# Kernel tuning notes

Hardware: AMD Instinct MI355X
Metric: run time of the kernel (lower is better)

Reference implementation:

```python
import jax, jax.numpy as jnp
import numpy as np

H = 512
N = 512
BSZ = 8
L = 4096
DIRECTION = 2  # 0=forward, 1=backward, 2=bidirectional (split N in half)


def setup_inputs() -> dict:
    key = jax.random.key(0)
    k = jax.random.split(key, 6)
    u = jax.random.normal(k[0], (BSZ, L, H), jnp.float32)
    # variable lengths in [L//2, L]
    lengths = jax.random.randint(k[1], (BSZ,), L // 2, L + 1).astype(jnp.int32)
    # LRU init: r_min=0, r_max=1, max_phase=2*pi
    u1 = jax.random.uniform(k[2], (N,), jnp.float32)
    nu_log = jnp.log(-0.5 * jnp.log(u1))
    u2 = jax.random.uniform(k[3], (N,), jnp.float32)
    theta_log = jnp.log(2.0 * np.pi * u2)
    lam = jnp.exp(-jnp.exp(nu_log) + 1j * jnp.exp(theta_log))  # (N,) complex
    gamma = jnp.sqrt(1.0 - jnp.abs(lam) ** 2)[:, None]          # (N,1)
    B = jax.random.normal(k[4], (H, N, 2), jnp.float32) / np.float32(np.sqrt(2 * H)) * gamma
    C = jax.random.normal(k[5], (2, H, N), jnp.float32) / np.float32(np.sqrt(N))
    return {"u": u, "lengths": lengths, "nu_log": nu_log, "theta_log": theta_log, "B": B, "C": C}


def _lru_scan(lam, Bu, reverse):
    """Diagonal linear recurrence x_t = lam * x_{t-1} + Bu_t along axis 2 via associative scan.
    lam: (n,) complex; Bu: (B, n, L) complex."""
    a = jnp.broadcast_to(lam[None, :, None], Bu.shape)

    def op(e1, e2):
        a1, b1 = e1
        a2, b2 = e2
        return a1 * a2, a2 * b1 + b2

    _, x = jax.lax.associative_scan(op, (a, Bu), axis=2, reverse=reverse)
    return x


def reference(u, lengths, nu_log, theta_log, B, C):
    lam = jnp.exp(-jnp.exp(nu_log) + 1j * jnp.exp(theta_log))  # (N,)
    Bc = B[..., 0] + 1j * B[..., 1]                            # (H, N) complex
    Bu = jnp.einsum('blh,hn->bnl', u, Bc)                      # (B, N, L) complex
    mask = jnp.arange(L)[None, :] < lengths[:, None]           # (B, L)
    Bu = Bu * mask[:, None, :]
    if DIRECTION == 2:
        h = N // 2
        x = jnp.concatenate([
            _lru_scan(lam[:h], Bu[:, :h], reverse=False),
            _lru_scan(lam[h:], Bu[:, h:], reverse=True),
        ], axis=1)
    elif DIRECTION == 0:
        x = _lru_scan(lam, Bu, reverse=False)
    else:
        x = _lru_scan(lam, Bu, reverse=True)
    x = x * mask[:, None, :]           # zero outputs past each sequence length
    x = jnp.swapaxes(x, 1, 2)          # (B, L, N)
    y = x.real @ C[0] - x.imag @ C[1]  # (B, L, H)  (requires H == N, as in source)
    return y
```

## Files before the change

### kernel.cpp

```cpp
#include <hip/hip_runtime.h>

#define L_SEQ   4096
#define BSZQ    8
#define ROWS    (BSZQ * L_SEQ)
#define KC1     512
#define NC1     1024
#define KC2     1024
#define NC2     512
#define CHUNK   64
#define NCHUNK  64

typedef __attribute__((ext_vector_type(8))) short bfrag;
typedef __attribute__((ext_vector_type(4))) float ffrag;

static __device__ __forceinline__ unsigned short f2bf(float f) {
    union { float f; unsigned int u; } v; v.f = f;
    unsigned int r = v.u + 0x7fffu + ((v.u >> 16) & 1u);
    return (unsigned short)(r >> 16);
}
static __device__ __forceinline__ unsigned int pk2(float a, float b) {
    return (unsigned int)f2bf(a) | ((unsigned int)f2bf(b) << 16);
}
static __device__ __forceinline__ float2 unpk2(unsigned int u) {
    union { unsigned int u; float f; } a, b;
    a.u = u << 16;
    b.u = u & 0xffff0000u;
    return make_float2(a.f, b.f);
}

static __device__ __forceinline__ void async16(const void* g, void* l) {
    __builtin_amdgcn_global_load_lds(
        (const __attribute__((address_space(1))) unsigned int*)g,
        (__attribute__((address_space(3))) unsigned int*)l,
        16, 0, 0);
}

__global__ __launch_bounds__(512) void lru_lam_kernel(
    const float* __restrict__ nu_log, const float* __restrict__ theta_log,
    float2* __restrict__ lam)
{
    int n = threadIdx.x;
    float mag = expf(-expf(nu_log[n]));
    float th  = expf(theta_log[n]);
    lam[n] = make_float2(mag * cosf(th), mag * sinf(th));
}

__global__ __launch_bounds__(256) void conv_mask_kernel(
    const float* __restrict__ u, const int* __restrict__ lengths,
    unsigned short* __restrict__ ub)
{
    int idx = blockIdx.x * 256 + threadIdx.x;
    int row = idx >> 6;
    int l = row & (L_SEQ - 1), b = row >> 12;
    bool keep = (l < lengths[b]);
    union { unsigned int s[4]; float4 f; } o;
    if (keep) {
        const float4 a = *(const float4*)(u + (size_t)idx * 8);
        const float4 c = *(const float4*)(u + (size_t)idx * 8 + 4);
        o.s[0] = pk2(a.x, a.y); o.s[1] = pk2(a.z, a.w);
        o.s[2] = pk2(c.x, c.y); o.s[3] = pk2(c.z, c.w);
    } else {
        o.s[0] = o.s[1] = o.s[2] = o.s[3] = 0u;
    }
    *(float4*)(ub + (size_t)idx * 8) = o.f;
}

__global__ __launch_bounds__(256) void prep_Bt_kernel(
    const float* __restrict__ B, unsigned short* __restrict__ Bt)
{
    int idx = blockIdx.x * 256 + threadIdx.x;
    int n2 = idx >> 9, h = idx & 511;
    Bt[idx] = f2bf(B[(size_t)h * 1024 + n2]);
}

__global__ __launch_bounds__(256) void prep_Dt_kernel(
    const float* __restrict__ C, unsigned short* __restrict__ Dt)
{
    int idx = blockIdx.x * 256 + threadIdx.x;
    int j = idx >> 10, k = idx & 1023;
    int n = k >> 1, c = k & 1;
    float v = C[((size_t)c * 512 + n) * 512 + j];
    Dt[idx] = f2bf(c ? -v : v);
}

template<int KD, int ND>
__global__ __launch_bounds__(256) void mfma_gemm_async(
    const unsigned short* __restrict__ A,
    const unsigned short* __restrict__ Bt,
    float* __restrict__ Co)
{
    __shared__ uint4 As[512];
    __shared__ uint4 Bs[512];
    const int tid  = threadIdx.x;
    const int row0 = blockIdx.x * 128;
    const int col0 = blockIdx.y * 128;
    const int lane = tid & 63, w = tid >> 6;
    const int q = lane >> 4, m16 = lane & 15;
    const int wr = (w >> 1) * 64, wc = (w & 1) * 64;

    ffrag acc[4][4];
#pragma unroll
    for (int i = 0; i < 4; i++)
#pragma unroll
        for (int j = 0; j < 4; j++) acc[i][j] = (ffrag)0.f;

    for (int kt = 0; kt < KD; kt += 32) {
#pragma unroll
        for (int i = 0; i < 2; i++) {
            int t = i * 256 + w * 64 + lane;
            int r = t >> 2, kq = t & 3;
            async16(A  + (size_t)(row0 + r) * KD + kt + kq * 8, &As[i * 256 + w * 64]);
            async16(Bt + (size_t)(col0 + r) * KD + kt + kq * 8, &Bs[i * 256 + w * 64]);
        }
        __syncthreads();

        bfrag a[4], b[4];
#pragma unroll
        for (int ri = 0; ri < 4; ri++)
            a[ri] = *(bfrag*)&As[(wr + ri * 16 + m16) * 4 + q];
#pragma unroll
        for (int ci = 0; ci < 4; ci++)
            b[ci] = *(bfrag*)&Bs[(wc + ci * 16 + m16) * 4 + q];
#pragma unroll
        for (int ri = 0; ri < 4; ri++)
#pragma unroll
            for (int ci = 0; ci < 4; ci++)
                acc[ri][ci] = __builtin_amdgcn_mfma_f32_16x16x32_bf16(
                    a[ri], b[ci], acc[ri][ci], 0, 0, 0);
        __syncthreads();
    }

#pragma unroll
    for (int ri = 0; ri < 4; ri++)
#pragma unroll
        for (int r4 = 0; r4 < 4; r4++) {
            int row = row0 + wr + ri * 16 + q * 4 + r4;
#pragma unroll
            for (int ci = 0; ci < 4; ci++) {
                int col = col0 + wc + ci * 16 + m16;
                Co[(size_t)row * ND + col] = acc[ri][ci][r4];
            }
        }
}

__global__ __launch_bounds__(512) void scan_local_kernel(
    const float2* __restrict__ bu, const float2* __restrict__ lam,
    unsigned int* __restrict__ buloc, float2* __restrict__ states)
{
    int n = threadIdx.x;
    int b = blockIdx.x >> 6;
    int c = blockIdx.x & 63;
    float2 lm = lam[n];
    float xr = 0.f, xi = 0.f;
    bool fwd = (n < 256);
    int l0 = fwd ? (c * CHUNK) : (c * CHUNK + CHUNK - 1);
    const float2* p = bu + ((size_t)b * L_SEQ + l0) * 512 + n;
    unsigned int* po = buloc + ((size_t)b * L_SEQ + l0) * 512 + n;
    ptrdiff_t step = fwd ? 512 : -512;
#pragma unroll 8
    for (int t = 0; t < CHUNK; t++) {
        float2 v = *p;
        float nr = lm.x * xr - lm.y * xi + v.x;
        float ni = lm.x * xi + lm.y * xr + v.y;
        xr = nr; xi = ni;
        *po = pk2(xr, xi);
        p += step; po += step;
    }
    states[((size_t)b * NCHUNK + c) * 512 + n] = make_float2(xr, xi);
}

__global__ __launch_bounds__(512) void scan_combine_kernel(
    const float2* __restrict__ states, float2* __restrict__ carries,
    const float2* __restrict__ lam)
{
    int n = threadIdx.x;
    int b = blockIdx.x;
    float2 lm = lam[n];
    float ar = lm.x, ai = lm.y;
#pragma unroll
    for (int i = 0; i < 6; i++) {
        float nr = ar * ar - ai * ai;
        ai = 2.f * ar * ai;
        ar = nr;
    }
    float cr = 0.f, ci = 0.f;
    bool fwd = (n < 256);
    if (fwd) {
        for (int c = 0; c < NCHUNK; c++) {
            size_t idx = ((size_t)b * NCHUNK + c) * 512 + n;
            carries[idx] = make_float2(cr, ci);
            float2 s = states[idx];
            float nr = ar * cr - ai * ci + s.x;
            float ni = ar * ci + ai * cr + s.y;
            cr = nr; ci = ni;
        }
    } else {
        for (int c = NCHUNK - 1; c >= 0; c--) {
            size_t idx = ((size_t)b * NCHUNK + c) * 512 + n;
            carries[idx] = make_float2(cr, ci);
            float2 s = states[idx];
            float nr = ar * cr - ai * ci + s.x;
            float ni = ar * ci + ai * cr + s.y;
            cr = nr; ci = ni;
        }
    }
}

__global__ __launch_bounds__(512) void scan_apply_kernel(
    unsigned int* __restrict__ buloc, const float2* __restrict__ carries,
    const float2* __restrict__ lam, const int* __restrict__ lengths)
{
    int n = threadIdx.x;
    int b = blockIdx.x >> 6;
    int c = blockIdx.x & 63;
    int len = lengths[b];
    float2 lm = lam[n];
    float2 cy = carries[((size_t)b * NCHUNK + c) * 512 + n];
    bool fwd = (n < 256);
    float pr = lm.x, pi = lm.y;
    int l0 = fwd ? (c * CHUNK) : (c * CHUNK + CHUNK - 1);
    int dl = fwd ? 1 : -1;
    unsigned int* p = buloc + ((size_t)b * L_SEQ + l0) * 512 + n;
    ptrdiff_t step = fwd ? 512 : -512;
    int l = l0;
#pragma unroll 8
    for (int t = 0; t < CHUNK; t++) {
        float2 v = unpk2(*p);
        float xr = v.x + pr * cy.x - pi * cy.y;
        float xi = v.y + pr * cy.y + pi * cy.x;
        if (l >= len) { xr = 0.f; xi = 0.f; }
        *p = pk2(xr, xi);
        float nr = pr * lm.x - pi * lm.y;
        pi = pr * lm.y + pi * lm.x;
        pr = nr;
        p += step; l += dl;
    }
}

extern "C" void kernel_launch(void* const* d_in, const int* in_sizes, int n_in,
                              void* d_out, int out_size, void* d_ws, size_t ws_size,
                              hipStream_t stream)
{
    const float* u        = (const float*)d_in[0];
    const int*   lengths  = (const int*)  d_in[1];
    const float* nu_log   = (const float*)d_in[2];
    const float* theta_log= (const float*)d_in[3];
    const float* B        = (const float*)d_in[4];
    const float* C        = (const float*)d_in[5];
    float* y = (float*)d_out;

    char* wp = (char*)d_ws;
    float2* lam     = (float2*)wp;  wp += 4096;
    float2* states  = (float2*)wp;  wp += (size_t)BSZQ * NCHUNK * 512 * 8;
    float2* carries = (float2*)wp;  wp += (size_t)BSZQ * NCHUNK * 512 * 8;
    float*  bu      = (float*)wp;   wp += (size_t)ROWS * 1024 * 4;
    unsigned short* ub = (unsigned short*)wp; wp += (size_t)ROWS * 512 * 2;
    unsigned int* buloc = (unsigned int*)wp;  wp += (size_t)ROWS * 512 * 4;
    unsigned short* Bt = (unsigned short*)wp; wp += (size_t)NC1 * KC1 * 2;
    unsigned short* Dt = (unsigned short*)wp; wp += (size_t)NC2 * KC2 * 2;

    lru_lam_kernel<<<1, 512, 0, stream>>>(nu_log, theta_log, lam);
    conv_mask_kernel<<<8192, 256, 0, stream>>>(u, lengths, ub);
    prep_Bt_kernel<<<2048, 256, 0, stream>>>(B, Bt);
    prep_Dt_kernel<<<2048, 256, 0, stream>>>(C, Dt);

    {
        dim3 grid(ROWS / 128, NC1 / 128);
        mfma_gemm_async<KC1, NC1><<<grid, 256, 0, stream>>>(ub, Bt, bu);
    }

    scan_local_kernel<<<BSZQ * NCHUNK, 512, 0, stream>>>(
        (const float2*)bu, lam, buloc, states);
    scan_combine_kernel<<<BSZQ, 512, 0, stream>>>(states, carries, lam);
    scan_apply_kernel<<<BSZQ * NCHUNK, 512, 0, stream>>>(
        buloc, carries, lam, lengths);

    {
        dim3 grid(ROWS / 128, NC2 / 128);
        mfma_gemm_async<KC2, NC2><<<grid, 256, 0, stream>>>(
            (const unsigned short*)buloc, Dt, y);
    }
}
```

Measured before the change: 315.7 us.

## Emit bf16 Bu from first GEMM and restructure scan as reduce-then-rescan

The first GEMM now stages its accumulator tile through shared memory and writes Bu as packed bf16 pairs instead of fp32, which halves that intermediate buffer. The local scan only computes chunk end states and no longer writes a separate local-scan buffer. The apply kernel reruns the recurrence from the carry and overwrites Bu in place with the final masked states. This removes one large fp32 write/read pass and a buffer, at the cost of redoing the recurrence and of bf16 rounding of Bu before the scan, which may reduce accuracy.

```diff
diff --git a/kernel.cpp b/kernel.cpp
--- a/kernel.cpp
+++ b/kernel.cpp
@@ -83,14 +83,17 @@
     Dt[idx] = f2bf(c ? -v : v);
 }
 
-template<int KD, int ND>
+template<int KD, int ND, bool BF16OUT>
 __global__ __launch_bounds__(256) void mfma_gemm_async(
     const unsigned short* __restrict__ A,
     const unsigned short* __restrict__ Bt,
-    float* __restrict__ Co)
-{
-    __shared__ uint4 As[512];
-    __shared__ uint4 Bs[512];
+    void* __restrict__ Co)
+{
+    __shared__ __align__(16) char smem[32 * 132 * 4];
+    uint4* As = (uint4*)smem;
+    uint4* Bs = As + 512;
+    float* Ts = (float*)smem;
+
     const int tid  = threadIdx.x;
     const int row0 = blockIdx.x * 128;
     const int col0 = blockIdx.y * 128;
@@ -130,22 +133,55 @@
         __syncthreads();
     }
 
-#pragma unroll
-    for (int ri = 0; ri < 4; ri++)
-#pragma unroll
-        for (int r4 = 0; r4 < 4; r4++) {
-            int row = row0 + wr + ri * 16 + q * 4 + r4;
-#pragma unroll
-            for (int ci = 0; ci < 4; ci++) {
-                int col = col0 + wc + ci * 16 + m16;
-                Co[(size_t)row * ND + col] = acc[ri][ci][r4];
+    if (BF16OUT) {
+        unsigned int* Cb = (unsigned int*)Co;
+        const int colc0 = col0 >> 1;
+#pragma unroll
+        for (int g = 0; g < 4; g++) {
+            if (g) __syncthreads();
+            if (wr == (g >> 1) * 64) {
+                int gw = g & 1;
+#pragma unroll
+                for (int rj = 0; rj < 2; rj++) {
+                    int ri = gw * 2 + rj;
+#pragma unroll
+                    for (int r4 = 0; r4 < 4; r4++) {
+                        int rsl = rj * 16 + q * 4 + r4;
+#pragma unroll
+                        for (int ci = 0; ci < 4; ci++)
+                            Ts[rsl * 132 + wc + ci * 16 + m16] = acc[ri][ci][r4];
+                    }
+                }
+            }
+            __syncthreads();
+#pragma unroll
+            for (int i = 0; i < 8; i++) {
+                int flat = i * 256 + tid;
+                int r = flat >> 6, cu = flat & 63;
+                float2 v = *(float2*)&Ts[r * 132 + cu * 2];
+                Cb[(size_t)(row0 + g * 32 + r) * (ND / 2) + colc0 + cu] =
+                    pk2(v.x, v.y);
             }
         }
-}
-
-__global__ __launch_bounds__(512) void scan_local_kernel(
-    const float2* __restrict__ bu, const float2* __restrict__ lam,
-    unsigned int* __restrict__ buloc, float2* __restrict__ states)
+    } else {
+        float* Cf = (float*)Co;
+#pragma unroll
+        for (int ri = 0; ri < 4; ri++)
+#pragma unroll
+            for (int r4 = 0; r4 < 4; r4++) {
+                int row = row0 + wr + ri * 16 + q * 4 + r4;
+#pragma unroll
+                for (int ci = 0; ci < 4; ci++) {
+                    int col = col0 + wc + ci * 16 + m16;
+                    Cf[(size_t)row * ND + col] = acc[ri][ci][r4];
+                }
+            }
+    }
+}
+
+__global__ __launch_bounds__(512) void scan_states_kernel(
+    const unsigned int* __restrict__ bu, const float2* __restrict__ lam,
+    float2* __restrict__ states)
 {
     int n = threadIdx.x;
     int b = blockIdx.x >> 6;
@@ -154,17 +190,15 @@
     float xr = 0.f, xi = 0.f;
     bool fwd = (n < 256);
     int l0 = fwd ? (c * CHUNK) : (c * CHUNK + CHUNK - 1);
-    const float2* p = bu + ((size_t)b * L_SEQ + l0) * 512 + n;
-    unsigned int* po = buloc + ((size_t)b * L_SEQ + l0) * 512 + n;
+    const unsigned int* p = bu + ((size_t)b * L_SEQ + l0) * 512 + n;
     ptrdiff_t step = fwd ? 512 : -512;
 #pragma unroll 8
     for (int t = 0; t < CHUNK; t++) {
-        float2 v = *p;
+        float2 v = unpk2(*p);
         float nr = lm.x * xr - lm.y * xi + v.x;
         float ni = lm.x * xi + lm.y * xr + v.y;
         xr = nr; xi = ni;
-        *po = pk2(xr, xi);
-        p += step; po += step;
+        p += step;
     }
     states[((size_t)b * NCHUNK + c) * 512 + n] = make_float2(xr, xi);
 }
@@ -207,7 +241,7 @@
 }
 
 __global__ __launch_bounds__(512) void scan_apply_kernel(
-    unsigned int* __restrict__ buloc, const float2* __restrict__ carries,
+    unsigned int* __restrict__ bu, const float2* __restrict__ carries,
     const float2* __restrict__ lam, const int* __restrict__ lengths)
 {
     int n = threadIdx.x;
@@ -217,22 +251,19 @@
     float2 lm = lam[n];
     float2 cy = carries[((size_t)b * NCHUNK + c) * 512 + n];
     bool fwd = (n < 256);
-    float pr = lm.x, pi = lm.y;
     int l0 = fwd ? (c * CHUNK) : (c * CHUNK + CHUNK - 1);
     int dl = fwd ? 1 : -1;
-    unsigned int* p = buloc + ((size_t)b * L_SEQ + l0) * 512 + n;
+    unsigned int* p = bu + ((size_t)b * L_SEQ + l0) * 512 + n;
     ptrdiff_t step = fwd ? 512 : -512;
+    float xr = cy.x, xi = cy.y;
     int l = l0;
 #pragma unroll 8
     for (int t = 0; t < CHUNK; t++) {
         float2 v = unpk2(*p);
-        float xr = v.x + pr * cy.x - pi * cy.y;
-        float xi = v.y + pr * cy.y + pi * cy.x;
-        if (l >= len) { xr = 0.f; xi = 0.f; }
-        *p = pk2(xr, xi);
-        float nr = pr * lm.x - pi * lm.y;
-        pi = pr * lm.y + pi * lm.x;
-        pr = nr;
+        float nr = lm.x * xr - lm.y * xi + v.x;
+        float ni = lm.x * xi + lm.y * xr + v.y;
+        xr = nr; xi = ni;
+        *p = (l >= len) ? 0u : pk2(xr, xi);
         p += step; l += dl;
     }
 }
@@ -253,9 +284,8 @@
     float2* lam     = (float2*)wp;  wp += 4096;
     float2* states  = (float2*)wp;  wp += (size_t)BSZQ * NCHUNK * 512 * 8;
     float2* carries = (float2*)wp;  wp += (size_t)BSZQ * NCHUNK * 512 * 8;
-    float*  bu      = (float*)wp;   wp += (size_t)ROWS * 1024 * 4;
+    unsigned int* bu = (unsigned int*)wp; wp += (size_t)ROWS * 512 * 4;
     unsigned short* ub = (unsigned short*)wp; wp += (size_t)ROWS * 512 * 2;
-    unsigned int* buloc = (unsigned int*)wp;  wp += (size_t)ROWS * 512 * 4;
     unsigned short* Bt = (unsigned short*)wp; wp += (size_t)NC1 * KC1 * 2;
     unsigned short* Dt = (unsigned short*)wp; wp += (size_t)NC2 * KC2 * 2;
 
@@ -266,18 +296,16 @@
 
     {
         dim3 grid(ROWS / 128, NC1 / 128);
-        mfma_gemm_async<KC1, NC1><<<grid, 256, 0, stream>>>(ub, Bt, bu);
-    }
-
-    scan_local_kernel<<<BSZQ * NCHUNK, 512, 0, stream>>>(
-        (const float2*)bu, lam, buloc, states);
+        mfma_gemm_async<KC1, NC1, true><<<grid, 256, 0, stream>>>(ub, Bt, bu);
+    }
+
+    scan_states_kernel<<<BSZQ * NCHUNK, 512, 0, stream>>>(bu, lam, states);
     scan_combine_kernel<<<BSZQ, 512, 0, stream>>>(states, carries, lam);
-    scan_apply_kernel<<<BSZQ * NCHUNK, 512, 0, stream>>>(
-        buloc, carries, lam, lengths);
+    scan_apply_kernel<<<BSZQ * NCHUNK, 512, 0, stream>>>(bu, carries, lam, lengths);
 
     {
         dim3 grid(ROWS / 128, NC2 / 128);
-        mfma_gemm_async<KC2, NC2><<<grid, 256, 0, stream>>>(
-            (const unsigned short*)buloc, Dt, y);
-    }
-}
+        mfma_gemm_async<KC2, NC2, false><<<grid, 256, 0, stream>>>(
+            (const unsigned short*)bu, Dt, y);
+    }
+}
```

Result: faster. 296.0 us (-6.2%).
